# Kernel tuning notes

Measured on AMD Instinct MI355X. Metric: run time of the kernel, lower is better.

## Reference

```python
import jax, jax.numpy as jnp
import numpy as np

VOCAB, EMB, HID, OUT = 32000, 512, 1024, 1
B, S = 128, 512


def setup_inputs() -> dict:
    key = jax.random.key(0)
    ks = jax.random.split(key, 8)
    x = jax.random.randint(ks[0], (B, S), 0, VOCAB, dtype=jnp.int64 if jax.config.jax_enable_x64 else jnp.int32)
    emb = jax.random.normal(ks[1], (VOCAB, EMB), dtype=jnp.float32)
    # torch Linear stores weight as [out, in], y = x @ W.T + b
    W_w = jax.random.normal(ks[2], (HID, EMB), dtype=jnp.float32) * (1.0 / np.sqrt(EMB))
    W_b = jax.random.normal(ks[3], (HID,), dtype=jnp.float32) * 0.01
    U_w = jax.random.normal(ks[4], (HID, HID), dtype=jnp.float32) * (1.0 / np.sqrt(HID))
    U_b = jax.random.normal(ks[5], (HID,), dtype=jnp.float32) * 0.01
    V_w = jax.random.normal(ks[6], (OUT, HID), dtype=jnp.float32) * (1.0 / np.sqrt(HID))
    V_b = jax.random.normal(ks[7], (OUT,), dtype=jnp.float32) * 0.01
    return {"x": x, "emb": emb, "W_w": W_w, "W_b": W_b, "U_w": U_w, "U_b": U_b, "V_w": V_w, "V_b": V_b}


def reference(x, emb, W_w, W_b, U_w, U_b, V_w, V_b):
    xe = emb[x]  # [B, S, E] embedding lookup
    # Precompute input projection for all timesteps (same math as per-step W(x_t))
    pre = jnp.einsum('bse,he->bsh', xe, W_w) + W_b  # [B, S, H]

    def step(h, p_t):
        # h_t = tanh(W x_t + b_W + U h_{t-1} + b_U)
        h_new = jnp.tanh(p_t + h @ U_w.T + U_b)
        return h_new, None

    h0 = jnp.zeros((x.shape[0], U_w.shape[0]), dtype=pre.dtype)
    hT, _ = jax.lax.scan(step, h0, jnp.swapaxes(pre, 0, 1))  # scan over seq
    logits = hT @ V_w.T + V_b  # [B, OUT]
    return jax.nn.sigmoid(logits)
```

## Files before the change

### kernel.cpp

```cpp
#include <hip/hip_runtime.h>
#include <hip/hip_bf16.h>

typedef short short8 __attribute__((ext_vector_type(8)));
typedef float f32x4 __attribute__((ext_vector_type(4)));

#define OFF_U   0x0UL
#define OFF_W   0x200000UL
#define OFF_PRE 0x300000UL
#define OFF_H0  0x8300000UL
#define OFF_H1  0x8340000UL
#define OFF_CNT 0x8380000UL

static __device__ __forceinline__ unsigned short f2bf(float f) {
  return __builtin_bit_cast(unsigned short, __float2bfloat16(f));
}
static __device__ __forceinline__ float bf2f(unsigned short u) {
  unsigned int v = (unsigned int)u << 16;
  return __builtin_bit_cast(float, v);
}
static __device__ __forceinline__ unsigned int pack2(float a, float b) {
  return (unsigned int)f2bf(a) | ((unsigned int)f2bf(b) << 16);
}
static __device__ __forceinline__ float fast_tanh(float x) {
  float xc = fminf(fmaxf(x, -10.f), 10.f);
  float e2 = __expf(2.f * xc);
  return 1.f - 2.f * __builtin_amdgcn_rcpf(e2 + 1.f);
}

__global__ __launch_bounds__(256) void cvt_bf16(const float* __restrict__ in,
                                                unsigned short* __restrict__ out, int n4) {
  int idx = blockIdx.x * 256 + threadIdx.x;
  if (idx < n4) {
    float4 v = *(const float4*)&in[idx * 4];
    uint2 p; p.x = pack2(v.x, v.y); p.y = pack2(v.z, v.w);
    *(uint2*)&out[idx * 4] = p;
  }
}

__global__ __launch_bounds__(256) void pre_gemm(const int* __restrict__ x,
                                                const float* __restrict__ emb,
                                                const unsigned short* __restrict__ Wbf,
                                                unsigned short* __restrict__ pre) {
  const int t   = blockIdx.y;
  const int n0  = blockIdx.x * 128;
  const int tid = threadIdx.x;
  const int lane = tid & 63, w = tid >> 6;
  const int q = lane >> 4, l15 = lane & 15;

  __shared__ unsigned short Alds[128][72];
  __shared__ unsigned short Blds[128][72];
  __shared__ int tok[128];
  if (tid < 128) tok[tid] = x[tid * 512 + t];
  __syncthreads();

  f32x4 acc[4][4];
  #pragma unroll
  for (int a = 0; a < 4; ++a)
    #pragma unroll
    for (int b = 0; b < 4; ++b) acc[a][b] = {0.f, 0.f, 0.f, 0.f};

  const int wm = (w & 1) * 64, wn = (w >> 1) * 64;

  for (int k0 = 0; k0 < 512; k0 += 64) {
    #pragma unroll
    for (int it = 0; it < 8; ++it) {
      int idx = it * 256 + tid;
      int r = idx >> 4, c4 = (idx & 15) * 4;
      float4 v = *(const float4*)&emb[tok[r] * 512 + k0 + c4];
      uint2 p; p.x = pack2(v.x, v.y); p.y = pack2(v.z, v.w);
      *(uint2*)&Alds[r][c4] = p;
    }
    #pragma unroll
    for (int it = 0; it < 4; ++it) {
      int idx = it * 256 + tid;
      int r = idx >> 3, c8 = (idx & 7) * 8;
      *(int4*)&Blds[r][c8] = *(const int4*)&Wbf[(n0 + r) * 512 + k0 + c8];
    }
    __syncthreads();
    #pragma unroll
    for (int kt = 0; kt < 2; ++kt) {
      short8 af[4], bfr[4];
      #pragma unroll
      for (int mt = 0; mt < 4; ++mt) af[mt]  = *(const short8*)&Alds[wm + mt*16 + l15][kt*32 + q*8];
      #pragma unroll
      for (int nt = 0; nt < 4; ++nt) bfr[nt] = *(const short8*)&Blds[wn + nt*16 + l15][kt*32 + q*8];
      #pragma unroll
      for (int mt = 0; mt < 4; ++mt)
        #pragma unroll
        for (int nt = 0; nt < 4; ++nt)
          acc[mt][nt] = __builtin_amdgcn_mfma_f32_16x16x32_bf16(af[mt], bfr[nt], acc[mt][nt], 0, 0, 0);
    }
    __syncthreads();
  }
  #pragma unroll
  for (int mt = 0; mt < 4; ++mt) {
    int brow = wm + mt * 16 + q * 4;
    #pragma unroll
    for (int nt = 0; nt < 4; ++nt) {
      int i = n0 + wn + nt * 16 + l15;
      #pragma unroll
      for (int r = 0; r < 4; ++r)
        pre[(t * 128 + brow + r) * 1024 + i] = f2bf(acc[mt][nt][r]);
    }
  }
}

__global__ __launch_bounds__(512, 2) void recurrence(const unsigned short* __restrict__ Ubf,
                                                     const unsigned short* __restrict__ pre,
                                                     const float* __restrict__ Wb,
                                                     const float* __restrict__ Ub,
                                                     unsigned short* __restrict__ h0buf,
                                                     unsigned short* __restrict__ h1buf,
                                                     unsigned int* __restrict__ cnt) {
  const int c   = blockIdx.x & 7;
  const int s   = blockIdx.x >> 3;
  const int tid = threadIdx.x;
  const int lane = tid & 63, wv = tid >> 6;
  const int q = lane >> 4, l15 = lane & 15;
  const int ibase = s * 128 + wv * 16;
  const int bglob = c * 16;

  __shared__ unsigned short hlds[16][1032];

  {
    int r = tid >> 5;
    int kk = (tid & 31) * 4;
    *(uint2*)&hlds[r][s * 128 + kk] = make_uint2(0u, 0u);
  }

  short8 A[32];
  {
    const unsigned short* Up = Ubf + (ibase + l15) * 1024 + q * 8;
    #pragma unroll
    for (int kt = 0; kt < 32; ++kt) A[kt] = *(const short8*)(Up + kt * 32);
  }
  #pragma unroll
  for (int kt = 0; kt < 32; ++kt) asm volatile("" : "+v"(A[kt]));

  float4 bias;
  {
    int i0 = ibase + q * 4;
    float4 wb = *(const float4*)&Wb[i0];
    float4 ub = *(const float4*)&Ub[i0];
    bias = make_float4(wb.x + ub.x, wb.y + ub.y, wb.z + ub.z, wb.w + ub.w);
  }

  unsigned int* fbase = cnt + c * 32;
  const bool pact = (lane < 8) && (lane != s);
  const unsigned int* fpoll = fbase + (lane & 7);
  unsigned int* fmine = fbase + s;
  const int sb = tid >> 7;
  const int sk = (tid & 127) * 8;
  const bool notown = (sk >> 7) != s;
  const unsigned short* prebase = pre + (size_t)(bglob + l15) * 1024 + ibase + q * 4;

  __syncthreads();

  #pragma unroll 1
  for (int t = 0; t < 512; ++t) {
    uint2 pvr;
    {
      const unsigned short* pp = prebase + (size_t)t * 131072;
      asm volatile("global_load_dwordx2 %0, %1, off" : "=v"(pvr) : "v"(pp));
    }

    const unsigned short* hprev = (t & 1) ? h1buf : h0buf;
    unsigned short* hnew        = (t & 1) ? h0buf : h1buf;
    const unsigned int et = (t == 0) ? 0u
                          : (((((t - 1) >> 1) & 1) ^ 1) ? 0x40004000u : 0u);

    if (t > 0) {
      if (wv == 0) {
        const unsigned int tt = (unsigned int)t;
        unsigned int va, vb;
        asm volatile("global_load_dword %0, %1, off sc1" : "=v"(va) : "v"(fpoll));
        for (;;) {
          asm volatile("global_load_dword %0, %1, off sc1\n\ts_waitcnt vmcnt(1)"
                       : "=v"(vb) : "v"(fpoll));
          unsigned int x = pact ? va : tt;
          if (__ballot(x < tt) == 0) break;
          asm volatile("global_load_dword %0, %1, off sc1\n\ts_waitcnt vmcnt(1)"
                       : "=v"(va) : "v"(fpoll));
          x = pact ? vb : tt;
          if (__ballot(x < tt) == 0) break;
        }
        asm volatile("s_waitcnt vmcnt(0)");
      }
      __syncthreads();
    }

    {
      const unsigned short* hp = hprev + (size_t)(bglob + sb) * 1024 + sk;
      int4 d0, d1, d2, d3;
      if (notown) {
        for (;;) {
          int4 r0, r1, r2, r3;
          asm volatile(
            "global_load_dwordx4 %0, %4, off sc1\n\t"
            "global_load_dwordx4 %1, %5, off sc1\n\t"
            "global_load_dwordx4 %2, %6, off sc1\n\t"
            "global_load_dwordx4 %3, %7, off sc1\n\t"
            "s_waitcnt vmcnt(0)"
            : "=&v"(r0), "=&v"(r1), "=&v"(r2), "=&v"(r3)
            : "v"(hp), "v"(hp + 4 * 1024), "v"(hp + 8 * 1024), "v"(hp + 12 * 1024));
          d0.x = r0.x ^ (int)et; d0.y = r0.y ^ (int)et; d0.z = r0.z ^ (int)et; d0.w = r0.w ^ (int)et;
          d1.x = r1.x ^ (int)et; d1.y = r1.y ^ (int)et; d1.z = r1.z ^ (int)et; d1.w = r1.w ^ (int)et;
          d2.x = r2.x ^ (int)et; d2.y = r2.y ^ (int)et; d2.z = r2.z ^ (int)et; d2.w = r2.w ^ (int)et;
          d3.x = r3.x ^ (int)et; d3.y = r3.y ^ (int)et; d3.z = r3.z ^ (int)et; d3.w = r3.w ^ (int)et;
          unsigned int bad = (unsigned int)(d0.x | d0.y | d0.z | d0.w |
                                            d1.x | d1.y | d1.z | d1.w |
                                            d2.x | d2.y | d2.z | d2.w |
                                            d3.x | d3.y | d3.z | d3.w) & 0x40004000u;
          if (bad == 0) break;
        }
        *(int4*)&hlds[sb][sk]      = d0;
        *(int4*)&hlds[sb + 4][sk]  = d1;
        *(int4*)&hlds[sb + 8][sk]  = d2;
        *(int4*)&hlds[sb + 12][sk] = d3;
      } else {
        asm volatile("s_waitcnt vmcnt(0)");
      }
    }
    __syncthreads();

    f32x4 acc0 = {0.f, 0.f, 0.f, 0.f}, acc1 = {0.f, 0.f, 0.f, 0.f};
    #pragma unroll
    for (int kt = 0; kt < 32; kt += 2) {
      short8 b0 = *(const short8*)&hlds[l15][kt * 32 + q * 8];
      short8 b1 = *(const short8*)&hlds[l15][kt * 32 + 32 + q * 8];
      acc0 = __builtin_amdgcn_mfma_f32_16x16x32_bf16(A[kt],     b0, acc0, 0, 0, 0);
      acc1 = __builtin_amdgcn_mfma_f32_16x16x32_bf16(A[kt + 1], b1, acc1, 0, 0, 0);
    }
    __syncthreads();

    float p0 = bf2f((unsigned short)(pvr.x & 0xffff));
    float p1 = bf2f((unsigned short)(pvr.x >> 16));
    float p2 = bf2f((unsigned short)(pvr.y & 0xffff));
    float p3 = bf2f((unsigned short)(pvr.y >> 16));
    float x0 = acc0[0] + acc1[0] + p0 + bias.x;
    float x1 = acc0[1] + acc1[1] + p1 + bias.y;
    float x2 = acc0[2] + acc1[2] + p2 + bias.z;
    float x3 = acc0[3] + acc1[3] + p3 + bias.w;
    uint2 pk;
    pk.x = pack2(fast_tanh(x0), fast_tanh(x1));
    pk.y = pack2(fast_tanh(x2), fast_tanh(x3));

    {
      const unsigned int tm = (((t >> 1) & 1) ^ 1) ? 0x40004000u : 0u;
      const int i0 = ibase + q * 4;
      *(uint2*)&hlds[l15][i0] = pk;
      uint2 pkt; pkt.x = pk.x ^ tm; pkt.y = pk.y ^ tm;
      unsigned short* dst = hnew + (size_t)(bglob + l15) * 1024 + i0;
      asm volatile("global_store_dwordx2 %0, %1, off sc1"
                   : : "v"(dst), "v"(pkt));
    }
    __syncthreads();
    if (tid == 0) {
      unsigned int tv = (unsigned int)(t + 1);
      asm volatile("global_store_dword %0, %1, off sc1" : : "v"(fmine), "v"(tv));
    }
  }
}

__global__ __launch_bounds__(64) void final_out(const unsigned short* __restrict__ hT,
                                                const float* __restrict__ Vw,
                                                const float* __restrict__ Vb,
                                                float* __restrict__ out) {
  int b = blockIdx.x, lane = threadIdx.x;
  float sum = 0.f;
  #pragma unroll
  for (int k = 0; k < 16; ++k) {
    int i = k * 64 + lane;
    sum += bf2f(hT[b * 1024 + i]) * Vw[i];
  }
  #pragma unroll
  for (int off = 32; off; off >>= 1) sum += __shfl_down(sum, off);
  if (lane == 0) out[b] = 1.f / (1.f + expf(-(sum + Vb[0])));
}

extern "C" void kernel_launch(void* const* d_in, const int* in_sizes, int n_in,
                              void* d_out, int out_size, void* d_ws, size_t ws_size,
                              hipStream_t stream) {
  const int*   x   = (const int*)d_in[0];
  const float* emb = (const float*)d_in[1];
  const float* W_w = (const float*)d_in[2];
  const float* W_b = (const float*)d_in[3];
  const float* U_w = (const float*)d_in[4];
  const float* U_b = (const float*)d_in[5];
  const float* V_w = (const float*)d_in[6];
  const float* V_b = (const float*)d_in[7];
  float* out = (float*)d_out;
  char*  ws  = (char*)d_ws;

  unsigned short* Ubf = (unsigned short*)(ws + OFF_U);
  unsigned short* Wbf = (unsigned short*)(ws + OFF_W);
  unsigned short* pre = (unsigned short*)(ws + OFF_PRE);
  unsigned short* h0  = (unsigned short*)(ws + OFF_H0);
  unsigned short* h1  = (unsigned short*)(ws + OFF_H1);
  unsigned int*   cnt = (unsigned int*)(ws + OFF_CNT);

  hipMemsetAsync(ws + OFF_H0, 0, (OFF_CNT - OFF_H0) + 0x1000, stream);

  cvt_bf16<<<1024, 256, 0, stream>>>(U_w, Ubf, 1024 * 1024 / 4);
  cvt_bf16<<<512, 256, 0, stream>>>(W_w, Wbf, 1024 * 512 / 4);

  pre_gemm<<<dim3(8, 512), 256, 0, stream>>>(x, emb, Wbf, pre);

  void* args[] = {&Ubf, &pre, &W_b, &U_b, &h0, &h1, &cnt};
  hipLaunchCooperativeKernel((void*)recurrence, dim3(64), dim3(512), args, 0, stream);

  final_out<<<128, 64, 0, stream>>>(h0, V_w, V_b, out);
}
```

Measured before the change: 1.589 ms.

## Interleave two batch groups per block to hide cross-block sync latency

Each recurrence block now handles two 16-row batch groups (A and B) with separate flag sets. It alternates between them so the wait for group B's peers overlaps with group A's compute and store, and vice versa. The grid is halved from 64 to 32 blocks, and the block's own h slice is kept in registers instead of re-read. In exchange each block does twice the serial work per step with extra barriers, and fewer CUs are in use.

```diff
diff --git a/kernel.cpp b/kernel.cpp
--- a/kernel.cpp
+++ b/kernel.cpp
@@ -105,6 +105,57 @@
   }
 }
 
+static __device__ __forceinline__ void poll_flags(const unsigned int* fp, unsigned int tt,
+                                                  bool pact) {
+  unsigned int va, vb;
+  asm volatile("global_load_dword %0, %1, off sc1" : "=v"(va) : "v"(fp));
+  for (;;) {
+    asm volatile("global_load_dword %0, %1, off sc1\n\ts_waitcnt vmcnt(1)"
+                 : "=v"(vb) : "v"(fp));
+    unsigned int x = pact ? va : tt;
+    if (__ballot(x < tt) == 0) break;
+    asm volatile("global_load_dword %0, %1, off sc1\n\ts_waitcnt vmcnt(1)"
+                 : "=v"(va) : "v"(fp));
+    x = pact ? vb : tt;
+    if (__ballot(x < tt) == 0) break;
+  }
+  asm volatile("s_waitcnt vmcnt(0)");
+}
+
+static __device__ __forceinline__ void stage_remote(const unsigned short* hp, unsigned int et,
+                                                    bool notown, int sb, int sk,
+                                                    unsigned short hlds[16][1032]) {
+  if (notown) {
+    int4 d0, d1, d2, d3;
+    for (;;) {
+      int4 r0, r1, r2, r3;
+      asm volatile(
+        "global_load_dwordx4 %0, %4, off sc1\n\t"
+        "global_load_dwordx4 %1, %5, off sc1\n\t"
+        "global_load_dwordx4 %2, %6, off sc1\n\t"
+        "global_load_dwordx4 %3, %7, off sc1\n\t"
+        "s_waitcnt vmcnt(0)"
+        : "=&v"(r0), "=&v"(r1), "=&v"(r2), "=&v"(r3)
+        : "v"(hp), "v"(hp + 4 * 1024), "v"(hp + 8 * 1024), "v"(hp + 12 * 1024));
+      d0.x = r0.x ^ (int)et; d0.y = r0.y ^ (int)et; d0.z = r0.z ^ (int)et; d0.w = r0.w ^ (int)et;
+      d1.x = r1.x ^ (int)et; d1.y = r1.y ^ (int)et; d1.z = r1.z ^ (int)et; d1.w = r1.w ^ (int)et;
+      d2.x = r2.x ^ (int)et; d2.y = r2.y ^ (int)et; d2.z = r2.z ^ (int)et; d2.w = r2.w ^ (int)et;
+      d3.x = r3.x ^ (int)et; d3.y = r3.y ^ (int)et; d3.z = r3.z ^ (int)et; d3.w = r3.w ^ (int)et;
+      unsigned int bad = (unsigned int)(d0.x | d0.y | d0.z | d0.w |
+                                        d1.x | d1.y | d1.z | d1.w |
+                                        d2.x | d2.y | d2.z | d2.w |
+                                        d3.x | d3.y | d3.z | d3.w) & 0x40004000u;
+      if (bad == 0) break;
+    }
+    *(int4*)&hlds[sb][sk]      = d0;
+    *(int4*)&hlds[sb + 4][sk]  = d1;
+    *(int4*)&hlds[sb + 8][sk]  = d2;
+    *(int4*)&hlds[sb + 12][sk] = d3;
+  } else {
+    asm volatile("s_waitcnt vmcnt(0)");
+  }
+}
+
 __global__ __launch_bounds__(512, 2) void recurrence(const unsigned short* __restrict__ Ubf,
                                                      const unsigned short* __restrict__ pre,
                                                      const float* __restrict__ Wb,
@@ -112,21 +163,16 @@
                                                      unsigned short* __restrict__ h0buf,
                                                      unsigned short* __restrict__ h1buf,
                                                      unsigned int* __restrict__ cnt) {
-  const int c   = blockIdx.x & 7;
-  const int s   = blockIdx.x >> 3;
+  const int c   = blockIdx.x & 3;
+  const int s   = blockIdx.x >> 2;
   const int tid = threadIdx.x;
   const int lane = tid & 63, wv = tid >> 6;
   const int q = lane >> 4, l15 = lane & 15;
   const int ibase = s * 128 + wv * 16;
-  const int bglob = c * 16;
+  const int bA = c * 32;
+  const int bB = c * 32 + 16;
 
   __shared__ unsigned short hlds[16][1032];
-
-  {
-    int r = tid >> 5;
-    int kk = (tid & 31) * 4;
-    *(uint2*)&hlds[r][s * 128 + kk] = make_uint2(0u, 0u);
-  }
 
   short8 A[32];
   {
@@ -145,119 +191,121 @@
     bias = make_float4(wb.x + ub.x, wb.y + ub.y, wb.z + ub.z, wb.w + ub.w);
   }
 
-  unsigned int* fbase = cnt + c * 32;
+  unsigned int* fbA = cnt + (c * 2 + 0) * 32;
+  unsigned int* fbB = cnt + (c * 2 + 1) * 32;
   const bool pact = (lane < 8) && (lane != s);
-  const unsigned int* fpoll = fbase + (lane & 7);
-  unsigned int* fmine = fbase + s;
+  const unsigned int* fpollA = fbA + (lane & 7);
+  const unsigned int* fpollB = fbB + (lane & 7);
+  unsigned int* fmineA = fbA + s;
+  unsigned int* fmineB = fbB + s;
   const int sb = tid >> 7;
   const int sk = (tid & 127) * 8;
   const bool notown = (sk >> 7) != s;
-  const unsigned short* prebase = pre + (size_t)(bglob + l15) * 1024 + ibase + q * 4;
-
-  __syncthreads();
+  const int i0 = ibase + q * 4;
+  const unsigned short* prebA = pre + (size_t)(bA + l15) * 1024 + i0;
+  const unsigned short* prebB = pre + (size_t)(bB + l15) * 1024 + i0;
+
+  uint2 pkA; pkA.x = 0u; pkA.y = 0u;
+  uint2 pkB; pkB.x = 0u; pkB.y = 0u;
 
   #pragma unroll 1
   for (int t = 0; t < 512; ++t) {
-    uint2 pvr;
-    {
-      const unsigned short* pp = prebase + (size_t)t * 131072;
-      asm volatile("global_load_dwordx2 %0, %1, off" : "=v"(pvr) : "v"(pp));
+    uint2 pvrA, pvrB;
+    {
+      const unsigned short* pp = prebA + (size_t)t * 131072;
+      asm volatile("global_load_dwordx2 %0, %1, off" : "=v"(pvrA) : "v"(pp));
+    }
+    {
+      const unsigned short* pp = prebB + (size_t)t * 131072;
+      asm volatile("global_load_dwordx2 %0, %1, off" : "=v"(pvrB) : "v"(pp));
     }
 
     const unsigned short* hprev = (t & 1) ? h1buf : h0buf;
     unsigned short* hnew        = (t & 1) ? h0buf : h1buf;
     const unsigned int et = (t == 0) ? 0u
                           : (((((t - 1) >> 1) & 1) ^ 1) ? 0x40004000u : 0u);
+    const unsigned int tm = (((t >> 1) & 1) ^ 1) ? 0x40004000u : 0u;
 
     if (t > 0) {
-      if (wv == 0) {
-        const unsigned int tt = (unsigned int)t;
-        unsigned int va, vb;
-        asm volatile("global_load_dword %0, %1, off sc1" : "=v"(va) : "v"(fpoll));
-        for (;;) {
-          asm volatile("global_load_dword %0, %1, off sc1\n\ts_waitcnt vmcnt(1)"
-                       : "=v"(vb) : "v"(fpoll));
-          unsigned int x = pact ? va : tt;
-          if (__ballot(x < tt) == 0) break;
-          asm volatile("global_load_dword %0, %1, off sc1\n\ts_waitcnt vmcnt(1)"
-                       : "=v"(va) : "v"(fpoll));
-          x = pact ? vb : tt;
-          if (__ballot(x < tt) == 0) break;
-        }
-        asm volatile("s_waitcnt vmcnt(0)");
+      if (wv == 0) poll_flags(fpollA, (unsigned int)t, pact);
+      __syncthreads();
+    }
+    {
+      const unsigned short* hp = hprev + (size_t)(bA + sb) * 1024 + sk;
+      stage_remote(hp, et, notown, sb, sk, hlds);
+      *(uint2*)&hlds[l15][i0] = pkA;
+    }
+    __syncthreads();
+
+    {
+      f32x4 acc0 = {0.f, 0.f, 0.f, 0.f}, acc1 = {0.f, 0.f, 0.f, 0.f};
+      #pragma unroll
+      for (int kt = 0; kt < 32; kt += 2) {
+        short8 b0 = *(const short8*)&hlds[l15][kt * 32 + q * 8];
+        short8 b1 = *(const short8*)&hlds[l15][kt * 32 + 32 + q * 8];
+        acc0 = __builtin_amdgcn_mfma_f32_16x16x32_bf16(A[kt],     b0, acc0, 0, 0, 0);
+        acc1 = __builtin_amdgcn_mfma_f32_16x16x32_bf16(A[kt + 1], b1, acc1, 0, 0, 0);
       }
-      __syncthreads();
-    }
-
-    {
-      const unsigned short* hp = hprev + (size_t)(bglob + sb) * 1024 + sk;
-      int4 d0, d1, d2, d3;
-      if (notown) {
-        for (;;) {
-          int4 r0, r1, r2, r3;
-          asm volatile(
-            "global_load_dwordx4 %0, %4, off sc1\n\t"
-            "global_load_dwordx4 %1, %5, off sc1\n\t"
-            "global_load_dwordx4 %2, %6, off sc1\n\t"
-            "global_load_dwordx4 %3, %7, off sc1\n\t"
-            "s_waitcnt vmcnt(0)"
-            : "=&v"(r0), "=&v"(r1), "=&v"(r2), "=&v"(r3)
-            : "v"(hp), "v"(hp + 4 * 1024), "v"(hp + 8 * 1024), "v"(hp + 12 * 1024));
-          d0.x = r0.x ^ (int)et; d0.y = r0.y ^ (int)et; d0.z = r0.z ^ (int)et; d0.w = r0.w ^ (int)et;
-          d1.x = r1.x ^ (int)et; d1.y = r1.y ^ (int)et; d1.z = r1.z ^ (int)et; d1.w = r1.w ^ (int)et;
-          d2.x = r2.x ^ (int)et; d2.y = r2.y ^ (int)et; d2.z = r2.z ^ (int)et; d2.w = r2.w ^ (int)et;
-          d3.x = r3.x ^ (int)et; d3.y = r3.y ^ (int)et; d3.z = r3.z ^ (int)et; d3.w = r3.w ^ (int)et;
-          unsigned int bad = (unsigned int)(d0.x | d0.y | d0.z | d0.w |
-                                            d1.x | d1.y | d1.z | d1.w |
-                                            d2.x | d2.y | d2.z | d2.w |
-                                            d3.x | d3.y | d3.z | d3.w) & 0x40004000u;
-          if (bad == 0) break;
-        }
-        *(int4*)&hlds[sb][sk]      = d0;
-        *(int4*)&hlds[sb + 4][sk]  = d1;
-        *(int4*)&hlds[sb + 8][sk]  = d2;
-        *(int4*)&hlds[sb + 12][sk] = d3;
-      } else {
-        asm volatile("s_waitcnt vmcnt(0)");
-      }
-    }
-    __syncthreads();
-
-    f32x4 acc0 = {0.f, 0.f, 0.f, 0.f}, acc1 = {0.f, 0.f, 0.f, 0.f};
-    #pragma unroll
-    for (int kt = 0; kt < 32; kt += 2) {
-      short8 b0 = *(const short8*)&hlds[l15][kt * 32 + q * 8];
-      short8 b1 = *(const short8*)&hlds[l15][kt * 32 + 32 + q * 8];
-      acc0 = __builtin_amdgcn_mfma_f32_16x16x32_bf16(A[kt],     b0, acc0, 0, 0, 0);
-      acc1 = __builtin_amdgcn_mfma_f32_16x16x32_bf16(A[kt + 1], b1, acc1, 0, 0, 0);
-    }
-    __syncthreads();
-
-    float p0 = bf2f((unsigned short)(pvr.x & 0xffff));
-    float p1 = bf2f((unsigned short)(pvr.x >> 16));
-    float p2 = bf2f((unsigned short)(pvr.y & 0xffff));
-    float p3 = bf2f((unsigned short)(pvr.y >> 16));
-    float x0 = acc0[0] + acc1[0] + p0 + bias.x;
-    float x1 = acc0[1] + acc1[1] + p1 + bias.y;
-    float x2 = acc0[2] + acc1[2] + p2 + bias.z;
-    float x3 = acc0[3] + acc1[3] + p3 + bias.w;
-    uint2 pk;
-    pk.x = pack2(fast_tanh(x0), fast_tanh(x1));
-    pk.y = pack2(fast_tanh(x2), fast_tanh(x3));
-
-    {
-      const unsigned int tm = (((t >> 1) & 1) ^ 1) ? 0x40004000u : 0u;
-      const int i0 = ibase + q * 4;
-      *(uint2*)&hlds[l15][i0] = pk;
-      uint2 pkt; pkt.x = pk.x ^ tm; pkt.y = pk.y ^ tm;
-      unsigned short* dst = hnew + (size_t)(bglob + l15) * 1024 + i0;
+      float p0 = bf2f((unsigned short)(pvrA.x & 0xffff));
+      float p1 = bf2f((unsigned short)(pvrA.x >> 16));
+      float p2 = bf2f((unsigned short)(pvrA.y & 0xffff));
+      float p3 = bf2f((unsigned short)(pvrA.y >> 16));
+      float x0 = acc0[0] + acc1[0] + p0 + bias.x;
+      float x1 = acc0[1] + acc1[1] + p1 + bias.y;
+      float x2 = acc0[2] + acc1[2] + p2 + bias.z;
+      float x3 = acc0[3] + acc1[3] + p3 + bias.w;
+      pkA.x = pack2(fast_tanh(x0), fast_tanh(x1));
+      pkA.y = pack2(fast_tanh(x2), fast_tanh(x3));
+      uint2 pkt; pkt.x = pkA.x ^ tm; pkt.y = pkA.y ^ tm;
+      unsigned short* dst = hnew + (size_t)(bA + l15) * 1024 + i0;
       asm volatile("global_store_dwordx2 %0, %1, off sc1"
                    : : "v"(dst), "v"(pkt));
     }
     __syncthreads();
     if (tid == 0) {
       unsigned int tv = (unsigned int)(t + 1);
-      asm volatile("global_store_dword %0, %1, off sc1" : : "v"(fmine), "v"(tv));
+      asm volatile("global_store_dword %0, %1, off sc1" : : "v"(fmineA), "v"(tv));
+    }
+
+    if (t > 0) {
+      if (wv == 0) poll_flags(fpollB, (unsigned int)t, pact);
+      __syncthreads();
+    }
+    {
+      const unsigned short* hp = hprev + (size_t)(bB + sb) * 1024 + sk;
+      stage_remote(hp, et, notown, sb, sk, hlds);
+      *(uint2*)&hlds[l15][i0] = pkB;
+    }
+    __syncthreads();
+
+    {
+      f32x4 acc0 = {0.f, 0.f, 0.f, 0.f}, acc1 = {0.f, 0.f, 0.f, 0.f};
+      #pragma unroll
+      for (int kt = 0; kt < 32; kt += 2) {
+        short8 b0 = *(const short8*)&hlds[l15][kt * 32 + q * 8];
+        short8 b1 = *(const short8*)&hlds[l15][kt * 32 + 32 + q * 8];
+        acc0 = __builtin_amdgcn_mfma_f32_16x16x32_bf16(A[kt],     b0, acc0, 0, 0, 0);
+        acc1 = __builtin_amdgcn_mfma_f32_16x16x32_bf16(A[kt + 1], b1, acc1, 0, 0, 0);
+      }
+      float p0 = bf2f((unsigned short)(pvrB.x & 0xffff));
+      float p1 = bf2f((unsigned short)(pvrB.x >> 16));
+      float p2 = bf2f((unsigned short)(pvrB.y & 0xffff));
+      float p3 = bf2f((unsigned short)(pvrB.y >> 16));
+      float x0 = acc0[0] + acc1[0] + p0 + bias.x;
+      float x1 = acc0[1] + acc1[1] + p1 + bias.y;
+      float x2 = acc0[2] + acc1[2] + p2 + bias.z;
+      float x3 = acc0[3] + acc1[3] + p3 + bias.w;
+      pkB.x = pack2(fast_tanh(x0), fast_tanh(x1));
+      pkB.y = pack2(fast_tanh(x2), fast_tanh(x3));
+      uint2 pkt; pkt.x = pkB.x ^ tm; pkt.y = pkB.y ^ tm;
+      unsigned short* dst = hnew + (size_t)(bB + l15) * 1024 + i0;
+      asm volatile("global_store_dwordx2 %0, %1, off sc1"
+                   : : "v"(dst), "v"(pkt));
+    }
+    __syncthreads();
+    if (tid == 0) {
+      unsigned int tv = (unsigned int)(t + 1);
+      asm volatile("global_store_dword %0, %1, off sc1" : : "v"(fmineB), "v"(tv));
     }
   }
 }
@@ -307,7 +355,7 @@
   pre_gemm<<<dim3(8, 512), 256, 0, stream>>>(x, emb, Wbf, pre);
 
   void* args[] = {&Ubf, &pre, &W_b, &U_b, &h0, &h1, &cnt};
-  hipLaunchCooperativeKernel((void*)recurrence, dim3(64), dim3(512), args, 0, stream);
+  hipLaunchCooperativeKernel((void*)recurrence, dim3(32), dim3(512), args, 0, stream);
 
   final_out<<<128, 64, 0, stream>>>(h0, V_w, V_b, out);
 }
```

Result: slower. 2.810 ms (+76.9%).

## Prefetch pre-activations two steps ahead and drop a barrier in recurrence loop

Applied to the files above, without the earlier changes.

The recurrence loop is unrolled by two with ping-pong registers, so each step's pre-activation load is issued two steps ahead instead of at the start of the same step. The h-exchange loads are issued once before the spin-check, so their latency overlaps with the pre-activation decode and prefetch. The block's own h slice is now written to LDS at the start of the next step rather than after the MFMA loop, which removes one __syncthreads per step. This reduces serialized latency on the per-step critical path, but relies on subtle vmcnt ordering between the inline-asm loads.

```diff
diff --git a/kernel.cpp b/kernel.cpp
--- a/kernel.cpp
+++ b/kernel.cpp
@@ -3,6 +3,7 @@
 
 typedef short short8 __attribute__((ext_vector_type(8)));
 typedef float f32x4 __attribute__((ext_vector_type(4)));
+typedef int   i32x4 __attribute__((ext_vector_type(4)));
 
 #define OFF_U   0x0UL
 #define OFF_W   0x200000UL
@@ -103,6 +104,23 @@
         pre[(t * 128 + brow + r) * 1024 + i] = f2bf(acc[mt][nt][r]);
     }
   }
+}
+
+static __device__ __forceinline__ void poll_flags(const unsigned int* fp, unsigned int tt,
+                                                  bool pact) {
+  unsigned int va, vb;
+  asm volatile("global_load_dword %0, %1, off sc1" : "=v"(va) : "v"(fp));
+  for (;;) {
+    asm volatile("global_load_dword %0, %1, off sc1\n\ts_waitcnt vmcnt(1)"
+                 : "=v"(vb) : "v"(fp));
+    unsigned int x = pact ? va : tt;
+    if (__ballot(x < tt) == 0) break;
+    asm volatile("global_load_dword %0, %1, off sc1\n\ts_waitcnt vmcnt(1)"
+                 : "=v"(va) : "v"(fp));
+    x = pact ? vb : tt;
+    if (__ballot(x < tt) == 0) break;
+  }
+  asm volatile("s_waitcnt vmcnt(0)");
 }
 
 __global__ __launch_bounds__(512, 2) void recurrence(const unsigned short* __restrict__ Ubf,
@@ -122,12 +140,6 @@
 
   __shared__ unsigned short hlds[16][1032];
 
-  {
-    int r = tid >> 5;
-    int kk = (tid & 31) * 4;
-    *(uint2*)&hlds[r][s * 128 + kk] = make_uint2(0u, 0u);
-  }
-
   short8 A[32];
   {
     const unsigned short* Up = Ubf + (ibase + l15) * 1024 + q * 8;
@@ -139,9 +151,9 @@
 
   float4 bias;
   {
-    int i0 = ibase + q * 4;
-    float4 wb = *(const float4*)&Wb[i0];
-    float4 ub = *(const float4*)&Ub[i0];
+    int i0b = ibase + q * 4;
+    float4 wb = *(const float4*)&Wb[i0b];
+    float4 ub = *(const float4*)&Ub[i0b];
     bias = make_float4(wb.x + ub.x, wb.y + ub.y, wb.z + ub.z, wb.w + ub.w);
   }
 
@@ -152,75 +164,84 @@
   const int sb = tid >> 7;
   const int sk = (tid & 127) * 8;
   const bool notown = (sk >> 7) != s;
-  const unsigned short* prebase = pre + (size_t)(bglob + l15) * 1024 + ibase + q * 4;
-
-  __syncthreads();
-
-  #pragma unroll 1
-  for (int t = 0; t < 512; ++t) {
-    uint2 pvr;
-    {
-      const unsigned short* pp = prebase + (size_t)t * 131072;
-      asm volatile("global_load_dwordx2 %0, %1, off" : "=v"(pvr) : "v"(pp));
-    }
-
+  const int i0 = ibase + q * 4;
+  const unsigned short* prebase = pre + (size_t)(bglob + l15) * 1024 + i0;
+
+  uint2 pk; pk.x = 0u; pk.y = 0u;
+
+  uint2 P0, P1;
+  {
+    const unsigned short* pp0 = prebase;
+    const unsigned short* pp1 = prebase + 131072;
+    asm volatile("global_load_dwordx2 %0, %1, off" : "=v"(P0) : "v"(pp0));
+    asm volatile("global_load_dwordx2 %0, %1, off" : "=v"(P1) : "v"(pp1));
+    asm volatile("s_waitcnt vmcnt(1)");
+    asm volatile("" : "+v"(P0));
+  }
+
+  auto body = [&](int t, uint2& Pcur, uint2& Pnxt) {
     const unsigned short* hprev = (t & 1) ? h1buf : h0buf;
     unsigned short* hnew        = (t & 1) ? h0buf : h1buf;
     const unsigned int et = (t == 0) ? 0u
                           : (((((t - 1) >> 1) & 1) ^ 1) ? 0x40004000u : 0u);
+    const unsigned int tm = (((t >> 1) & 1) ^ 1) ? 0x40004000u : 0u;
 
     if (t > 0) {
-      if (wv == 0) {
-        const unsigned int tt = (unsigned int)t;
-        unsigned int va, vb;
-        asm volatile("global_load_dword %0, %1, off sc1" : "=v"(va) : "v"(fpoll));
-        for (;;) {
-          asm volatile("global_load_dword %0, %1, off sc1\n\ts_waitcnt vmcnt(1)"
-                       : "=v"(vb) : "v"(fpoll));
-          unsigned int x = pact ? va : tt;
-          if (__ballot(x < tt) == 0) break;
-          asm volatile("global_load_dword %0, %1, off sc1\n\ts_waitcnt vmcnt(1)"
-                       : "=v"(va) : "v"(fpoll));
-          x = pact ? vb : tt;
-          if (__ballot(x < tt) == 0) break;
-        }
-        asm volatile("s_waitcnt vmcnt(0)");
+      if (wv == 0) poll_flags(fpoll, (unsigned int)t, pact);
+      __syncthreads();
+    }
+
+    const unsigned short* hp = hprev + (size_t)(bglob + sb) * 1024 + sk;
+    i32x4 r0, r1, r2, r3;
+    if (notown) {
+      asm volatile(
+        "global_load_dwordx4 %0, %4, off sc1\n\t"
+        "global_load_dwordx4 %1, %5, off sc1\n\t"
+        "global_load_dwordx4 %2, %6, off sc1\n\t"
+        "global_load_dwordx4 %3, %7, off sc1"
+        : "=&v"(r0), "=&v"(r1), "=&v"(r2), "=&v"(r3)
+        : "v"(hp), "v"(hp + 4 * 1024), "v"(hp + 8 * 1024), "v"(hp + 12 * 1024));
+    }
+    float p0 = bf2f((unsigned short)(Pcur.x & 0xffff));
+    float p1 = bf2f((unsigned short)(Pcur.x >> 16));
+    float p2 = bf2f((unsigned short)(Pcur.y & 0xffff));
+    float p3 = bf2f((unsigned short)(Pcur.y >> 16));
+    {
+      int tp = (t + 2 < 512) ? (t + 2) : 510;
+      const unsigned short* pp = prebase + (size_t)tp * 131072;
+      asm volatile("global_load_dwordx2 %0, %1, off" : "=v"(Pcur) : "v"(pp));
+    }
+    asm volatile("s_waitcnt vmcnt(1)");
+    asm volatile("" : "+v"(Pnxt));
+    if (notown) {
+      asm volatile("" : "+v"(r0));
+      asm volatile("" : "+v"(r1));
+      asm volatile("" : "+v"(r2));
+      asm volatile("" : "+v"(r3));
+      i32x4 d0, d1, d2, d3;
+      for (;;) {
+        d0 = r0 ^ (int)et;
+        d1 = r1 ^ (int)et;
+        d2 = r2 ^ (int)et;
+        d3 = r3 ^ (int)et;
+        i32x4 o = d0 | d1 | d2 | d3;
+        unsigned int bad = (unsigned int)(o.x | o.y | o.z | o.w) & 0x40004000u;
+        if (bad == 0) break;
+        asm volatile(
+          "global_load_dwordx4 %0, %4, off sc1\n\t"
+          "global_load_dwordx4 %1, %5, off sc1\n\t"
+          "global_load_dwordx4 %2, %6, off sc1\n\t"
+          "global_load_dwordx4 %3, %7, off sc1\n\t"
+          "s_waitcnt vmcnt(0)"
+          : "=&v"(r0), "=&v"(r1), "=&v"(r2), "=&v"(r3)
+          : "v"(hp), "v"(hp + 4 * 1024), "v"(hp + 8 * 1024), "v"(hp + 12 * 1024));
       }
-      __syncthreads();
-    }
-
-    {
-      const unsigned short* hp = hprev + (size_t)(bglob + sb) * 1024 + sk;
-      int4 d0, d1, d2, d3;
-      if (notown) {
-        for (;;) {
-          int4 r0, r1, r2, r3;
-          asm volatile(
-            "global_load_dwordx4 %0, %4, off sc1\n\t"
-            "global_load_dwordx4 %1, %5, off sc1\n\t"
-            "global_load_dwordx4 %2, %6, off sc1\n\t"
-            "global_load_dwordx4 %3, %7, off sc1\n\t"
-            "s_waitcnt vmcnt(0)"
-            : "=&v"(r0), "=&v"(r1), "=&v"(r2), "=&v"(r3)
-            : "v"(hp), "v"(hp + 4 * 1024), "v"(hp + 8 * 1024), "v"(hp + 12 * 1024));
-          d0.x = r0.x ^ (int)et; d0.y = r0.y ^ (int)et; d0.z = r0.z ^ (int)et; d0.w = r0.w ^ (int)et;
-          d1.x = r1.x ^ (int)et; d1.y = r1.y ^ (int)et; d1.z = r1.z ^ (int)et; d1.w = r1.w ^ (int)et;
-          d2.x = r2.x ^ (int)et; d2.y = r2.y ^ (int)et; d2.z = r2.z ^ (int)et; d2.w = r2.w ^ (int)et;
-          d3.x = r3.x ^ (int)et; d3.y = r3.y ^ (int)et; d3.z = r3.z ^ (int)et; d3.w = r3.w ^ (int)et;
-          unsigned int bad = (unsigned int)(d0.x | d0.y | d0.z | d0.w |
-                                            d1.x | d1.y | d1.z | d1.w |
-                                            d2.x | d2.y | d2.z | d2.w |
-                                            d3.x | d3.y | d3.z | d3.w) & 0x40004000u;
-          if (bad == 0) break;
-        }
-        *(int4*)&hlds[sb][sk]      = d0;
-        *(int4*)&hlds[sb + 4][sk]  = d1;
-        *(int4*)&hlds[sb + 8][sk]  = d2;
-        *(int4*)&hlds[sb + 12][sk] = d3;
-      } else {
-        asm volatile("s_waitcnt vmcnt(0)");
-      }
-    }
+      *(i32x4*)&hlds[sb][sk]      = d0;
+      *(i32x4*)&hlds[sb + 4][sk]  = d1;
+      *(i32x4*)&hlds[sb + 8][sk]  = d2;
+      *(i32x4*)&hlds[sb + 12][sk] = d3;
+    }
+    *(uint2*)&hlds[l15][i0] = pk;
     __syncthreads();
 
     f32x4 acc0 = {0.f, 0.f, 0.f, 0.f}, acc1 = {0.f, 0.f, 0.f, 0.f};
@@ -231,24 +252,14 @@
       acc0 = __builtin_amdgcn_mfma_f32_16x16x32_bf16(A[kt],     b0, acc0, 0, 0, 0);
       acc1 = __builtin_amdgcn_mfma_f32_16x16x32_bf16(A[kt + 1], b1, acc1, 0, 0, 0);
     }
-    __syncthreads();
-
-    float p0 = bf2f((unsigned short)(pvr.x & 0xffff));
-    float p1 = bf2f((unsigned short)(pvr.x >> 16));
-    float p2 = bf2f((unsigned short)(pvr.y & 0xffff));
-    float p3 = bf2f((unsigned short)(pvr.y >> 16));
+
     float x0 = acc0[0] + acc1[0] + p0 + bias.x;
     float x1 = acc0[1] + acc1[1] + p1 + bias.y;
     float x2 = acc0[2] + acc1[2] + p2 + bias.z;
     float x3 = acc0[3] + acc1[3] + p3 + bias.w;
-    uint2 pk;
     pk.x = pack2(fast_tanh(x0), fast_tanh(x1));
     pk.y = pack2(fast_tanh(x2), fast_tanh(x3));
-
     {
-      const unsigned int tm = (((t >> 1) & 1) ^ 1) ? 0x40004000u : 0u;
-      const int i0 = ibase + q * 4;
-      *(uint2*)&hlds[l15][i0] = pk;
       uint2 pkt; pkt.x = pk.x ^ tm; pkt.y = pk.y ^ tm;
       unsigned short* dst = hnew + (size_t)(bglob + l15) * 1024 + i0;
       asm volatile("global_store_dwordx2 %0, %1, off sc1"
@@ -259,6 +270,12 @@
       unsigned int tv = (unsigned int)(t + 1);
       asm volatile("global_store_dword %0, %1, off sc1" : : "v"(fmine), "v"(tv));
     }
+  };
+
+  #pragma unroll 1
+  for (int t = 0; t < 512; t += 2) {
+    body(t,     P0, P1);
+    body(t + 1, P1, P0);
   }
 }
 
```

Measured after the change: 1.623 ms. 1.02x slower.

## Use per-wavefront progress flags instead of block barrier before flag store

Applied to the files above, without the earlier changes.

Each wavefront now publishes its own step counter right after its h-store, and the pollers check all 64 flags (8 slices × 8 waves) per batch group. This removes the block-wide __syncthreads before signalling, so a finished wave signals without waiting for slower siblings. The cost is more flag memory and a wider poll per step. The change also switches the xor/or validity check to vector types, which is cosmetic.

```diff
diff --git a/kernel.cpp b/kernel.cpp
--- a/kernel.cpp
+++ b/kernel.cpp
@@ -3,6 +3,7 @@
 
 typedef short short8 __attribute__((ext_vector_type(8)));
 typedef float f32x4 __attribute__((ext_vector_type(4)));
+typedef int   i32x4 __attribute__((ext_vector_type(4)));
 
 #define OFF_U   0x0UL
 #define OFF_W   0x200000UL
@@ -103,6 +104,23 @@
         pre[(t * 128 + brow + r) * 1024 + i] = f2bf(acc[mt][nt][r]);
     }
   }
+}
+
+static __device__ __forceinline__ void poll_flags(const unsigned int* fp, unsigned int tt,
+                                                  bool pact) {
+  unsigned int va, vb;
+  asm volatile("global_load_dword %0, %1, off sc1" : "=v"(va) : "v"(fp));
+  for (;;) {
+    asm volatile("global_load_dword %0, %1, off sc1\n\ts_waitcnt vmcnt(1)"
+                 : "=v"(vb) : "v"(fp));
+    unsigned int x = pact ? va : tt;
+    if (__ballot(x < tt) == 0) break;
+    asm volatile("global_load_dword %0, %1, off sc1\n\ts_waitcnt vmcnt(1)"
+                 : "=v"(va) : "v"(fp));
+    x = pact ? vb : tt;
+    if (__ballot(x < tt) == 0) break;
+  }
+  asm volatile("s_waitcnt vmcnt(0)");
 }
 
 __global__ __launch_bounds__(512, 2) void recurrence(const unsigned short* __restrict__ Ubf,
@@ -145,10 +163,10 @@
     bias = make_float4(wb.x + ub.x, wb.y + ub.y, wb.z + ub.z, wb.w + ub.w);
   }
 
-  unsigned int* fbase = cnt + c * 32;
-  const bool pact = (lane < 8) && (lane != s);
-  const unsigned int* fpoll = fbase + (lane & 7);
-  unsigned int* fmine = fbase + s;
+  unsigned int* fbase = cnt + c * 64;
+  const bool pact = (lane >> 3) != s;
+  const unsigned int* fpoll = fbase + lane;
+  unsigned int* fmine = fbase + s * 8 + wv;
   const int sb = tid >> 7;
   const int sk = (tid & 127) * 8;
   const bool notown = (sk >> 7) != s;
@@ -170,31 +188,16 @@
                           : (((((t - 1) >> 1) & 1) ^ 1) ? 0x40004000u : 0u);
 
     if (t > 0) {
-      if (wv == 0) {
-        const unsigned int tt = (unsigned int)t;
-        unsigned int va, vb;
-        asm volatile("global_load_dword %0, %1, off sc1" : "=v"(va) : "v"(fpoll));
-        for (;;) {
-          asm volatile("global_load_dword %0, %1, off sc1\n\ts_waitcnt vmcnt(1)"
-                       : "=v"(vb) : "v"(fpoll));
-          unsigned int x = pact ? va : tt;
-          if (__ballot(x < tt) == 0) break;
-          asm volatile("global_load_dword %0, %1, off sc1\n\ts_waitcnt vmcnt(1)"
-                       : "=v"(va) : "v"(fpoll));
-          x = pact ? vb : tt;
-          if (__ballot(x < tt) == 0) break;
-        }
-        asm volatile("s_waitcnt vmcnt(0)");
-      }
+      if (wv == 0) poll_flags(fpoll, (unsigned int)t, pact);
       __syncthreads();
     }
 
     {
       const unsigned short* hp = hprev + (size_t)(bglob + sb) * 1024 + sk;
-      int4 d0, d1, d2, d3;
+      i32x4 d0, d1, d2, d3;
       if (notown) {
         for (;;) {
-          int4 r0, r1, r2, r3;
+          i32x4 r0, r1, r2, r3;
           asm volatile(
             "global_load_dwordx4 %0, %4, off sc1\n\t"
             "global_load_dwordx4 %1, %5, off sc1\n\t"
@@ -203,20 +206,18 @@
             "s_waitcnt vmcnt(0)"
             : "=&v"(r0), "=&v"(r1), "=&v"(r2), "=&v"(r3)
             : "v"(hp), "v"(hp + 4 * 1024), "v"(hp + 8 * 1024), "v"(hp + 12 * 1024));
-          d0.x = r0.x ^ (int)et; d0.y = r0.y ^ (int)et; d0.z = r0.z ^ (int)et; d0.w = r0.w ^ (int)et;
-          d1.x = r1.x ^ (int)et; d1.y = r1.y ^ (int)et; d1.z = r1.z ^ (int)et; d1.w = r1.w ^ (int)et;
-          d2.x = r2.x ^ (int)et; d2.y = r2.y ^ (int)et; d2.z = r2.z ^ (int)et; d2.w = r2.w ^ (int)et;
-          d3.x = r3.x ^ (int)et; d3.y = r3.y ^ (int)et; d3.z = r3.z ^ (int)et; d3.w = r3.w ^ (int)et;
-          unsigned int bad = (unsigned int)(d0.x | d0.y | d0.z | d0.w |
-                                            d1.x | d1.y | d1.z | d1.w |
-                                            d2.x | d2.y | d2.z | d2.w |
-                                            d3.x | d3.y | d3.z | d3.w) & 0x40004000u;
+          d0 = r0 ^ (int)et;
+          d1 = r1 ^ (int)et;
+          d2 = r2 ^ (int)et;
+          d3 = r3 ^ (int)et;
+          i32x4 o = d0 | d1 | d2 | d3;
+          unsigned int bad = (unsigned int)(o.x | o.y | o.z | o.w) & 0x40004000u;
           if (bad == 0) break;
         }
-        *(int4*)&hlds[sb][sk]      = d0;
-        *(int4*)&hlds[sb + 4][sk]  = d1;
-        *(int4*)&hlds[sb + 8][sk]  = d2;
-        *(int4*)&hlds[sb + 12][sk] = d3;
+        *(i32x4*)&hlds[sb][sk]      = d0;
+        *(i32x4*)&hlds[sb + 4][sk]  = d1;
+        *(i32x4*)&hlds[sb + 8][sk]  = d2;
+        *(i32x4*)&hlds[sb + 12][sk] = d3;
       } else {
         asm volatile("s_waitcnt vmcnt(0)");
       }
@@ -254,8 +255,7 @@
       asm volatile("global_store_dwordx2 %0, %1, off sc1"
                    : : "v"(dst), "v"(pkt));
     }
-    __syncthreads();
-    if (tid == 0) {
+    if (lane == 0) {
       unsigned int tv = (unsigned int)(t + 1);
       asm volatile("global_store_dword %0, %1, off sc1" : : "v"(fmine), "v"(tv));
     }
```

Measured after the change: 2.261 ms. 42.3% more time.
